# Kernel tuning notes

Hardware: AMD Instinct MI355X
Metric: run time of the kernel (lower is better)

## Reference

```python
import jax, jax.numpy as jnp
import numpy as np

HIDDEN = 2048
VOCAB = 32768
SEQ = 4608
N_CHUNKS = 9
CAP = 30.0
IGNORE = -100


def setup_inputs() -> dict:
    key = jax.random.key(0)
    k1, k2, k3 = jax.random.split(key, 3)
    weight = (jax.random.normal(k1, (VOCAB, HIDDEN), dtype=jnp.float32) * 0.02).astype(jnp.bfloat16)
    hidden = jax.random.normal(k2, (1, SEQ, HIDDEN), dtype=jnp.float32)
    input_ids = jax.random.randint(k3, (1, SEQ), 0, VOCAB)
    attention_mask = jnp.ones((1, SEQ), dtype=jnp.int32)
    return {"weight": weight, "hidden": hidden, "input_ids": input_ids,
            "attention_mask": attention_mask}


def _build_labels(input_ids, attention_mask):
    # labels[t] = input_ids[t+1], masked-out positions and the final position -> -100
    ids = input_ids[0]
    am = attention_mask[0]
    lab = jnp.where(am[1:] == 0, IGNORE, ids[1:])            # [S-1]
    lab = jnp.concatenate([lab, jnp.full((1,), IGNORE, lab.dtype)])  # [S]
    return lab


def reference(weight, hidden, input_ids, attention_mask):
    labels = _build_labels(input_ids, attention_mask)        # [S]
    x = hidden.reshape(-1, HIDDEN)                           # [S, H] fp32
    chunk = SEQ // N_CHUNKS
    xs = x.reshape(N_CHUNKS, chunk, HIDDEN)
    ls = labels.reshape(N_CHUNKS, chunk)

    wT = weight.T                                            # [H, V] bf16

    def chunk_loss(args):
        xc, lc = args                                        # [c,H], [c]
        # softcapped logits: CAP * tanh((x @ W^T) / CAP), mm in bf16
        t = jnp.tanh((xc.astype(jnp.bfloat16) @ wT) / CAP).astype(jnp.float32)  # [c,V]
        z = CAP * (t - jnp.max(t, axis=1, keepdims=True))    # stable shifted logits
        logp = z - jnp.log(jnp.sum(jnp.exp(z), axis=1, keepdims=True))
        valid = lc != IGNORE
        idx = jnp.where(valid, lc, 0)
        nll = -jnp.take_along_axis(logp, idx[:, None], axis=1)[:, 0]
        return jnp.sum(jnp.where(valid, nll, 0.0))

    losses = jax.lax.map(chunk_loss, (xs, ls))               # [N_CHUNKS]
    return jnp.sum(losses)
```

## Files before the change

### kernel.cpp

```cpp
#include <hip/hip_runtime.h>
#include <hip/hip_bf16.h>
#include <cstdint>

#define S_LEN   4608
#define HID     2048
#define VOCAB_N 32768
#define CAPV    30.0f
#define IGNORE_IDX (-100)
#define NT512   512
#define NKT     32

typedef short bf16x8 __attribute__((ext_vector_type(8)));
typedef float f32x4  __attribute__((ext_vector_type(4)));

__device__ __forceinline__ unsigned short f2bf_rtne(float f) {
    unsigned int u = __float_as_uint(f);
    unsigned int r = u + 0x7fffu + ((u >> 16) & 1u);
    return (unsigned short)(r >> 16);
}
__device__ __forceinline__ float bfr(float f) {
    unsigned int u = __float_as_uint(f);
    unsigned int r = u + 0x7fffu + ((u >> 16) & 1u);
    return __uint_as_float(r & 0xffff0000u);
}
__device__ __forceinline__ float bf_lo(unsigned int u) { return __uint_as_float(u << 16); }
__device__ __forceinline__ float bf_hi(unsigned int u) { return __uint_as_float(u & 0xffff0000u); }
__device__ __forceinline__ float bfdot2(unsigned int x, unsigned int w) {
    return bf_lo(x) * bf_lo(w) + bf_hi(x) * bf_hi(w);
}
__device__ __forceinline__ float softcap_ref(float logit) {
    float lb = bfr(logit);
    float x  = bfr(lb / CAPV);
    float e  = __expf(2.0f * x);
    float t  = bfr((e - 1.0f) / (e + 1.0f));
    return CAPV * t;
}

__global__ void cvt_kernel(const float* __restrict__ h, unsigned short* __restrict__ xb,
                           float* __restrict__ out) {
    if (blockIdx.x == 0 && threadIdx.x == 0) out[0] = 0.0f;
    int i = blockIdx.x * blockDim.x + threadIdx.x;
    float4 v = ((const float4*)h)[i];
    ushort4 o;
    o.x = f2bf_rtne(v.x); o.y = f2bf_rtne(v.y);
    o.z = f2bf_rtne(v.z); o.w = f2bf_rtne(v.w);
    ((ushort4*)xb)[i] = o;
}

__global__ __launch_bounds__(512, 2)
void gemm_lse_kernel(const unsigned short* __restrict__ X,
                     const unsigned short* __restrict__ W,
                     float* __restrict__ partL) {
    __shared__ __align__(16) unsigned short As[2][256 * 64];
    __shared__ __align__(16) unsigned short Bs[2][256 * 64];

    const int tid  = threadIdx.x;
    const int wid  = tid >> 6;
    const int lane = tid & 63;
    const int wr   = wid >> 2;
    const int wc   = wid & 3;
    const int q    = lane >> 4, l16 = lane & 15;
    const int tileM = blockIdx.x * 256;
    const int tileN = blockIdx.y * 256;

    const int srow = lane >> 3;
    const int csrc = (lane & 7) ^ srow;
    const unsigned short* Ag = X + (size_t)(tileM + wid * 8 + srow) * HID + csrc * 8;
    const unsigned short* Wg = W + (size_t)(tileN + wid * 8 + srow) * HID + csrc * 8;

    const int abase = (wr * 128 + l16) * 64;
    const int bbase = (wc * 64  + l16) * 64;
    const int koff0 = ((q    ) ^ (l16 & 7)) * 8;
    const int koff1 = ((q + 4) ^ (l16 & 7)) * 8;

    bf16x8 av[8][2], bv[4][2];
    f32x4  acc[8][4] = {};

#define STAGE_A(BUF, H, KT) do {                                                          \
    const unsigned short* _g = Ag + (size_t)(H) * 128 * HID + (size_t)(KT) * 64;          \
    __builtin_amdgcn_global_load_lds(                                                     \
        (const __attribute__((address_space(1))) void*)_g,                                \
        (__attribute__((address_space(3))) void*)&As[BUF][((H) * 128 + wid * 8) * 64],    \
        16, 0, 0);                                                                        \
    __builtin_amdgcn_global_load_lds(                                                     \
        (const __attribute__((address_space(1))) void*)(_g + (size_t)64 * HID),           \
        (__attribute__((address_space(3))) void*)&As[BUF][((H) * 128 + 64 + wid * 8) * 64],\
        16, 0, 0);                                                                        \
} while (0)

#define STAGE_B(BUF, H, KT) do {                                                          \
    const unsigned short* _g = Wg + (size_t)(H) * 128 * HID + (size_t)(KT) * 64;          \
    __builtin_amdgcn_global_load_lds(                                                     \
        (const __attribute__((address_space(1))) void*)_g,                                \
        (__attribute__((address_space(3))) void*)&Bs[BUF][((H) * 128 + wid * 8) * 64],    \
        16, 0, 0);                                                                        \
    __builtin_amdgcn_global_load_lds(                                                     \
        (const __attribute__((address_space(1))) void*)(_g + (size_t)64 * HID),           \
        (__attribute__((address_space(3))) void*)&Bs[BUF][((H) * 128 + 64 + wid * 8) * 64],\
        16, 0, 0);                                                                        \
} while (0)

#define LDA(BUF, MH) do {                                                                 \
    _Pragma("unroll") for (int fm = 0; fm < 4; ++fm) {                                    \
        av[(MH) * 4 + fm][0] = *(const bf16x8*)&As[BUF][abase + ((MH) * 64 + fm * 16) * 64 + koff0]; \
        av[(MH) * 4 + fm][1] = *(const bf16x8*)&As[BUF][abase + ((MH) * 64 + fm * 16) * 64 + koff1]; \
    } } while (0)

#define LDB(BUF, NH) do {                                                                 \
    _Pragma("unroll") for (int fn = 0; fn < 2; ++fn) {                                    \
        bv[(NH) * 2 + fn][0] = *(const bf16x8*)&Bs[BUF][bbase + ((NH) * 32 + fn * 16) * 64 + koff0]; \
        bv[(NH) * 2 + fn][1] = *(const bf16x8*)&Bs[BUF][bbase + ((NH) * 32 + fn * 16) * 64 + koff1]; \
    } } while (0)

#define MFMAQ(MH, NH) do {                                                                \
    _Pragma("unroll") for (int kk = 0; kk < 2; ++kk)                                      \
    _Pragma("unroll") for (int fm = 0; fm < 4; ++fm)                                      \
    _Pragma("unroll") for (int fn = 0; fn < 2; ++fn)                                      \
        acc[(MH) * 4 + fm][(NH) * 2 + fn] = __builtin_amdgcn_mfma_f32_16x16x32_bf16(      \
            av[(MH) * 4 + fm][kk], bv[(NH) * 2 + fn][kk],                                 \
            acc[(MH) * 4 + fm][(NH) * 2 + fn], 0, 0, 0);                                  \
} while (0)

#define BAR()   __builtin_amdgcn_s_barrier()
#define PRIO1() __builtin_amdgcn_s_setprio(1)
#define PRIO0() __builtin_amdgcn_s_setprio(0)
#define VMCNT4() asm volatile("s_waitcnt vmcnt(4)" ::: "memory")
#define VMCNT0() asm volatile("s_waitcnt vmcnt(0)" ::: "memory")

#define KTILE(CUR, NXT, T) do {                                                           \
    LDA(CUR, 0); LDB(CUR, 0); STAGE_B(NXT, 0, (T) + 1);                                   \
    BAR(); PRIO1(); MFMAQ(0, 0); PRIO0(); BAR();                                          \
    LDA(CUR, 1); LDB(CUR, 1); STAGE_B(NXT, 1, (T) + 1);                                   \
    BAR(); PRIO1(); MFMAQ(0, 1); PRIO0(); BAR();                                          \
    STAGE_A(CUR, 0, (T) + 2);                                                             \
    BAR(); PRIO1(); MFMAQ(1, 0); PRIO0(); BAR();                                          \
    STAGE_A(CUR, 1, (T) + 2);                                                             \
    BAR(); PRIO1(); MFMAQ(1, 1); PRIO0();                                                 \
    VMCNT4(); BAR();                                                                      \
} while (0)

    STAGE_A(0, 0, 0); STAGE_A(0, 1, 0);
    STAGE_B(0, 0, 0); STAGE_B(0, 1, 0);
    STAGE_A(1, 0, 1); STAGE_A(1, 1, 1);
    VMCNT4();
    BAR();

    #pragma unroll 1
    for (int t = 0; t < NKT - 2; t += 2) {
        KTILE(0, 1, t);
        KTILE(1, 0, t + 1);
    }

    LDA(0, 0); LDB(0, 0); STAGE_B(1, 0, 31);
    BAR(); PRIO1(); MFMAQ(0, 0); PRIO0(); BAR();
    LDA(0, 1); LDB(0, 1); STAGE_B(1, 1, 31);
    BAR(); PRIO1(); MFMAQ(0, 1); PRIO0(); BAR();
    BAR(); PRIO1(); MFMAQ(1, 0); PRIO0(); BAR();
    PRIO1(); MFMAQ(1, 1); PRIO0();
    VMCNT0(); BAR();

    LDA(1, 0); LDB(1, 0);
    PRIO1(); MFMAQ(0, 0); PRIO0();
    LDA(1, 1); LDB(1, 1);
    PRIO1(); MFMAQ(0, 1); PRIO0();
    PRIO1(); MFMAQ(1, 0); PRIO0();
    PRIO1(); MFMAQ(1, 1); PRIO0();

    const int rowbase = tileM + wr * 128;
    const int ntile   = blockIdx.y * 4 + wc;
    #pragma unroll
    for (int m = 0; m < 8; ++m) {
        #pragma unroll
        for (int r = 0; r < 4; ++r) {
            float s = 0.0f;
            #pragma unroll
            for (int n = 0; n < 4; ++n)
                s += __expf(softcap_ref(acc[m][n][r]));
            s += __shfl_xor(s, 1);
            s += __shfl_xor(s, 2);
            s += __shfl_xor(s, 4);
            s += __shfl_xor(s, 8);
            if (l16 == 0)
                partL[(size_t)(rowbase + m * 16 + q * 4 + r) * NT512 + ntile] = s;
        }
    }

#undef STAGE_A
#undef STAGE_B
#undef LDA
#undef LDB
#undef MFMAQ
#undef BAR
#undef PRIO1
#undef PRIO0
#undef VMCNT4
#undef VMCNT0
#undef KTILE
}

__global__ void row_reduce_kernel(const unsigned short* __restrict__ X,
                                  const unsigned short* __restrict__ W,
                                  const int* __restrict__ ids,
                                  const int* __restrict__ am,
                                  const float* __restrict__ partL,
                                  float* __restrict__ out) {
    __shared__ float blk[4];
    const int wave = threadIdx.x >> 6;
    const int lane = threadIdx.x & 63;
    const int r = blockIdx.x * 4 + wave;

    int lab = IGNORE_IDX;
    if (r < S_LEN - 1 && am[r + 1] != 0) lab = ids[r + 1];
    const bool valid = (lab >= 0 && lab < VOCAB_N);

    float dot = 0.0f;
    if (valid) {
        const unsigned short* xr = X + (size_t)r   * HID;
        const unsigned short* wr = W + (size_t)lab * HID;
        #pragma unroll
        for (int c = 0; c < 4; ++c) {
            const int off = c * 512 + lane * 8;
            uint4 xu = *(const uint4*)(xr + off);
            uint4 wu = *(const uint4*)(wr + off);
            dot += bfdot2(xu.x, wu.x) + bfdot2(xu.y, wu.y) +
                   bfdot2(xu.z, wu.z) + bfdot2(xu.w, wu.w);
        }
    }
    #pragma unroll
    for (int m = 1; m < 64; m <<= 1) dot += __shfl_xor(dot, m);

    float L = 0.0f;
    const float* pr = partL + (size_t)r * NT512;
    #pragma unroll
    for (int i = 0; i < 8; ++i) L += pr[i * 64 + lane];
    #pragma unroll
    for (int m = 1; m < 64; m <<= 1) L += __shfl_xor(L, m);

    if (lane == 0) {
        float loss = 0.0f;
        if (valid) loss = logf(L) - softcap_ref(dot);
        blk[wave] = loss;
    }
    __syncthreads();
    if (threadIdx.x == 0)
        atomicAdd(out, blk[0] + blk[1] + blk[2] + blk[3]);
}

extern "C" void kernel_launch(void* const* d_in, const int* in_sizes, int n_in,
                              void* d_out, int out_size, void* d_ws, size_t ws_size,
                              hipStream_t stream) {
    const unsigned short* W  = (const unsigned short*)d_in[0];
    const float*  hidden     = (const float*)d_in[1];
    const int*    ids        = (const int*)d_in[2];
    const int*    am         = (const int*)d_in[3];
    float* out = (float*)d_out;

    char* ws = (char*)d_ws;
    unsigned short* Xb = (unsigned short*)ws;
    float* partL       = (float*)(ws + (size_t)S_LEN * HID * 2);

    cvt_kernel<<<(S_LEN * HID / 4) / 256, 256, 0, stream>>>(hidden, Xb, out);

    dim3 g(S_LEN / 256, VOCAB_N / 256);
    gemm_lse_kernel<<<g, 512, 0, stream>>>(Xb, W, partL);

    row_reduce_kernel<<<S_LEN / 4, 256, 0, stream>>>(Xb, W, ids, am, partL, out);
}
```

Measured before the change: 1.091 ms.

## Software-pipeline LDS fragment reads one quadrant ahead of MFMA in GEMM k-loop

Restructures the k-tile schedule so that LDS-to-register reads for the next MFMA quadrant, including the first quadrant of the next k-tile, are issued before the current quadrant's MFMAs. This lets LDS read latency overlap with matrix math instead of stalling at the start of each quadrant. The vmcnt waits are moved earlier and split into finer steps (vmcnt 4, then vmcnt 2) so the next buffer is resident before it is read ahead. The epilogue is reworked to match. The cost is more register pressure from holding fragments for two quadrants at once, and a tighter ordering of barriers against global-to-LDS loads.

```diff
diff --git a/kernel.cpp b/kernel.cpp
--- a/kernel.cpp
+++ b/kernel.cpp
@@ -100,13 +100,13 @@
         16, 0, 0);                                                                        \
 } while (0)
 
-#define LDA(BUF, MH) do {                                                                 \
+#define RD_A(BUF, MH) do {                                                                \
     _Pragma("unroll") for (int fm = 0; fm < 4; ++fm) {                                    \
         av[(MH) * 4 + fm][0] = *(const bf16x8*)&As[BUF][abase + ((MH) * 64 + fm * 16) * 64 + koff0]; \
         av[(MH) * 4 + fm][1] = *(const bf16x8*)&As[BUF][abase + ((MH) * 64 + fm * 16) * 64 + koff1]; \
     } } while (0)
 
-#define LDB(BUF, NH) do {                                                                 \
+#define RD_B(BUF, NH) do {                                                                \
     _Pragma("unroll") for (int fn = 0; fn < 2; ++fn) {                                    \
         bv[(NH) * 2 + fn][0] = *(const bf16x8*)&Bs[BUF][bbase + ((NH) * 32 + fn * 16) * 64 + koff0]; \
         bv[(NH) * 2 + fn][1] = *(const bf16x8*)&Bs[BUF][bbase + ((NH) * 32 + fn * 16) * 64 + koff1]; \
@@ -125,18 +125,18 @@
 #define PRIO1() __builtin_amdgcn_s_setprio(1)
 #define PRIO0() __builtin_amdgcn_s_setprio(0)
 #define VMCNT4() asm volatile("s_waitcnt vmcnt(4)" ::: "memory")
+#define VMCNT2() asm volatile("s_waitcnt vmcnt(2)" ::: "memory")
 #define VMCNT0() asm volatile("s_waitcnt vmcnt(0)" ::: "memory")
 
 #define KTILE(CUR, NXT, T) do {                                                           \
-    LDA(CUR, 0); LDB(CUR, 0); STAGE_B(NXT, 0, (T) + 1);                                   \
+    RD_B(CUR, 1); STAGE_B(NXT, 0, (T) + 1);                                               \
     BAR(); PRIO1(); MFMAQ(0, 0); PRIO0(); BAR();                                          \
-    LDA(CUR, 1); LDB(CUR, 1); STAGE_B(NXT, 1, (T) + 1);                                   \
-    BAR(); PRIO1(); MFMAQ(0, 1); PRIO0(); BAR();                                          \
-    STAGE_A(CUR, 0, (T) + 2);                                                             \
-    BAR(); PRIO1(); MFMAQ(1, 0); PRIO0(); BAR();                                          \
-    STAGE_A(CUR, 1, (T) + 2);                                                             \
-    BAR(); PRIO1(); MFMAQ(1, 1); PRIO0();                                                 \
-    VMCNT4(); BAR();                                                                      \
+    RD_A(CUR, 1); STAGE_B(NXT, 1, (T) + 1);                                               \
+    BAR(); PRIO1(); MFMAQ(0, 1); PRIO0(); VMCNT4(); BAR();                                \
+    RD_A(NXT, 0); STAGE_A(CUR, 0, (T) + 2);                                               \
+    BAR(); PRIO1(); MFMAQ(1, 0); PRIO0(); VMCNT2(); BAR();                                \
+    RD_B(NXT, 0); STAGE_A(CUR, 1, (T) + 2);                                               \
+    BAR(); PRIO1(); MFMAQ(1, 1); PRIO0(); BAR();                                          \
 } while (0)
 
     STAGE_A(0, 0, 0); STAGE_A(0, 1, 0);
@@ -144,6 +144,7 @@
     STAGE_A(1, 0, 1); STAGE_A(1, 1, 1);
     VMCNT4();
     BAR();
+    RD_A(0, 0); RD_B(0, 0);
 
     #pragma unroll 1
     for (int t = 0; t < NKT - 2; t += 2) {
@@ -151,17 +152,18 @@
         KTILE(1, 0, t + 1);
     }
 
-    LDA(0, 0); LDB(0, 0); STAGE_B(1, 0, 31);
+    RD_B(0, 1); STAGE_B(1, 0, 31);
     BAR(); PRIO1(); MFMAQ(0, 0); PRIO0(); BAR();
-    LDA(0, 1); LDB(0, 1); STAGE_B(1, 1, 31);
-    BAR(); PRIO1(); MFMAQ(0, 1); PRIO0(); BAR();
-    BAR(); PRIO1(); MFMAQ(1, 0); PRIO0(); BAR();
-    PRIO1(); MFMAQ(1, 1); PRIO0();
-    VMCNT0(); BAR();
-
-    LDA(1, 0); LDB(1, 0);
+    RD_A(0, 1); STAGE_B(1, 1, 31);
+    BAR(); PRIO1(); MFMAQ(0, 1); PRIO0(); VMCNT4(); BAR();
+    RD_A(1, 0);
+    BAR(); PRIO1(); MFMAQ(1, 0); PRIO0(); VMCNT0(); BAR();
+    RD_B(1, 0);
+    BAR(); PRIO1(); MFMAQ(1, 1); PRIO0(); BAR();
+
+    RD_B(1, 1);
     PRIO1(); MFMAQ(0, 0); PRIO0();
-    LDA(1, 1); LDB(1, 1);
+    RD_A(1, 1);
     PRIO1(); MFMAQ(0, 1); PRIO0();
     PRIO1(); MFMAQ(1, 0); PRIO0();
     PRIO1(); MFMAQ(1, 1); PRIO0();
@@ -187,13 +189,14 @@
 
 #undef STAGE_A
 #undef STAGE_B
-#undef LDA
-#undef LDB
+#undef RD_A
+#undef RD_B
 #undef MFMAQ
 #undef BAR
 #undef PRIO1
 #undef PRIO0
 #undef VMCNT4
+#undef VMCNT2
 #undef VMCNT0
 #undef KTILE
 }
```

Result: faster. 1.057 ms (-3.1%).
